# Optimization experiments

Hardware: AMD Instinct MI355X
Metric: run time of the kernel (lower is better)

## Reference

```python
import jax, jax.numpy as jnp
import numpy as np

N_NODES = 100000
N_EDGES = 3200000
IN_FEATS = 512
EDGE_FEATS = 24
OUT_FEATS = 512
LN_EPS = 1e-5


def setup_inputs() -> dict:
    key = jax.random.key(0)
    ks = jax.random.split(key, 8)
    h = jax.random.normal(ks[0], (N_NODES, IN_FEATS), dtype=jnp.float32)
    m = jax.random.normal(ks[1], (N_EDGES, EDGE_FEATS), dtype=jnp.float32)
    dst = jax.random.randint(ks[2], (N_EDGES,), 0, N_NODES, dtype=jnp.int32)
    norm = jax.random.uniform(ks[3], (N_NODES, 1), dtype=jnp.float32)
    stdv = 1.0 / np.sqrt(IN_FEATS + EDGE_FEATS)
    W = jax.random.uniform(ks[4], (OUT_FEATS, IN_FEATS + EDGE_FEATS), dtype=jnp.float32, minval=-stdv, maxval=stdv)
    b = jax.random.uniform(ks[5], (OUT_FEATS,), dtype=jnp.float32, minval=-stdv, maxval=stdv)
    gamma = jnp.ones((OUT_FEATS,), dtype=jnp.float32)
    beta = jnp.zeros((OUT_FEATS,), dtype=jnp.float32)
    return {"h": h, "m": m, "dst": dst, "norm": norm, "W": W, "b": b, "gamma": gamma, "beta": beta}


def reference(h, m, dst, norm, W, b, gamma, beta):
    # copy_e + sum: segment-sum edge features into destination nodes -> [N, 24]
    ah = jax.ops.segment_sum(m, dst, num_segments=N_NODES)
    # scale by per-node norm, concat with node features -> [N, in+24]
    x = jnp.concatenate([h, ah * norm], axis=1)
    # linear
    y = jnp.einsum('nd,od->no', x, W) + b
    # layernorm (elementwise affine)
    mu = jnp.mean(y, axis=-1, keepdims=True)
    var = jnp.mean((y - mu) ** 2, axis=-1, keepdims=True)
    y = gamma * (y - mu) * jax.lax.rsqrt(var + LN_EPS) + beta
    # activation = relu
    return jax.nn.relu(y)
```

## Files before the change

### kernel.cpp

```cpp
#include <hip/hip_runtime.h>
#include <hip/hip_bf16.h>
#include <stdint.h>

#define NN 100000
#define NE 3200000
#define EF 24
#define KF 536
#define BM 64

typedef __attribute__((ext_vector_type(8))) short bf16x8;
typedef __attribute__((ext_vector_type(4))) float f32x4;

__device__ __forceinline__ unsigned short f2bf(float f) {
  union { float f; unsigned int u; } v; v.f = f;
  unsigned int r = v.u + 0x7FFFu + ((v.u >> 16) & 1u);
  return (unsigned short)(r >> 16);
}

__device__ __forceinline__ void gload_lds16(const void* g, void* l) {
  __builtin_amdgcn_global_load_lds(
      (const __attribute__((address_space(1))) unsigned int*)g,
      (__attribute__((address_space(3))) unsigned int*)l, 16, 0, 0);
}

__global__ void wconv_kernel(const float* __restrict__ W, unsigned short* __restrict__ Wb) {
  int i = blockIdx.x * blockDim.x + threadIdx.x;
  if (i >= 17 * 32 * 64 * 8) return;
  int j = i & 7;
  int lane = (i >> 3) & 63;
  int nt = (i >> 9) & 31;
  int kt = i >> 14;
  int row = nt * 16 + (lane & 15);
  int k = kt * 32 + (lane >> 4) * 8 + j;
  float v = (k < KF) ? W[row * KF + k] : 0.0f;
  Wb[i] = f2bf(v);
}

__global__ __launch_bounds__(256) void init_u64_kernel(unsigned long long* __restrict__ acc) {
  int i = blockIdx.x * 256 + threadIdx.x;
  if (i < NN * 6) acc[i] = 0x4000400040004000ULL;
}

__global__ __launch_bounds__(256) void scatter_u64_kernel(
    const float* __restrict__ m, const int* __restrict__ dst,
    unsigned long long* __restrict__ acc) {
  int i = blockIdx.x * 256 + threadIdx.x;
  if (i >= NE * 6) return;
  int e = i / 6;
  int fp = i - e * 6;
  float4 v = *(const float4*)(m + (size_t)e * EF + fp * 4);
  long long a0 = (long long)__float2int_rn(v.x * 128.f);
  long long a1 = (long long)__float2int_rn(v.y * 128.f);
  long long a2 = (long long)__float2int_rn(v.z * 128.f);
  long long a3 = (long long)__float2int_rn(v.w * 128.f);
  unsigned long long add = (unsigned long long)(a0 + (a1 << 16) + (a2 << 32) + (a3 << 48));
  atomicAdd(acc + (size_t)dst[e] * 6 + fp, add);
}

__global__ __launch_bounds__(256) void decode_u64_kernel(
    const unsigned long long* __restrict__ acc, const float* __restrict__ norm,
    float* __restrict__ ah) {
  int i = blockIdx.x * 256 + threadIdx.x;
  if (i >= NN * 6) return;
  int n = i / 6;
  unsigned long long x = acc[i];
  float nv = norm[n] * (1.0f / 128.0f);
  float4 o;
  o.x = (float)((int)((x >> 0) & 0xFFFF) - 16384) * nv;
  o.y = (float)((int)((x >> 16) & 0xFFFF) - 16384) * nv;
  o.z = (float)((int)((x >> 32) & 0xFFFF) - 16384) * nv;
  o.w = (float)((int)((x >> 48) & 0xFFFF) - 16384) * nv;
  *(float4*)(ah + (size_t)i * 4) = o;
}

__global__ __launch_bounds__(512, 4) void gemm_ln_kernel(
    const float* __restrict__ h, const float* __restrict__ ah,
    const unsigned short* __restrict__ Wb,
    const float* __restrict__ bias, const float* __restrict__ gamma,
    const float* __restrict__ beta, float* __restrict__ out) {
  __shared__ __align__(16) unsigned short Alds[4 * 4 * 16 * 8];
  __shared__ __align__(16) unsigned short Blds[32 * 4 * 16 * 8];
  __shared__ float red[4][BM][2];
  __shared__ float stats[BM][2];

  const int t = threadIdx.x;
  const int lane = t & 63;
  const int w = t >> 6;
  const int lgrp = lane >> 4;
  const int llow = lane & 15;
  const int mg = w >> 2;
  const int ng = w & 3;
  const int blockRow = blockIdx.x * BM;

  const int am = t >> 3;
  const int akg = (t >> 1) & 3;
  const int ahalf = t & 1;
  const int arow = blockRow + am;
  char* aldsdst = (char*)Alds + (((am >> 4) * 64 + akg * 16 + (am & 15)) * 16 + ahalf * 8);

  f32x4 acc[2][8];
#pragma unroll
  for (int i = 0; i < 2; ++i)
#pragma unroll
    for (int j = 0; j < 8; ++j) acc[i][j] = (f32x4){0.f, 0.f, 0.f, 0.f};

  float4 ra = make_float4(0.f, 0.f, 0.f, 0.f);
  if (arow < NN) ra = *(const float4*)(h + (size_t)arow * 512 + akg * 8 + ahalf * 4);

  for (int kt = 0; kt < 17; ++kt) {
    {
      const unsigned short* src = Wb + ((size_t)(kt * 32 + w) * 64 + lane) * 8;
#pragma unroll
      for (int j = 0; j < 4; ++j)
        gload_lds16(src + (size_t)j * 8 * 64 * 8, (char*)Blds + (j * 8 + w) * 1024);
    }
    {
      ushort4 bv;
      bv.x = f2bf(ra.x); bv.y = f2bf(ra.y); bv.z = f2bf(ra.z); bv.w = f2bf(ra.w);
      *(ushort4*)aldsdst = bv;
    }
    ra = make_float4(0.f, 0.f, 0.f, 0.f);
    if (kt < 16 && arow < NN) {
      if (kt < 15) {
        ra = *(const float4*)(h + (size_t)arow * 512 + (kt + 1) * 32 + akg * 8 + ahalf * 4);
      } else if (akg < 3) {
        ra = *(const float4*)(ah + (size_t)arow * EF + akg * 8 + ahalf * 4);
      }
    }
    __syncthreads();

    bf16x8 af0 = *(const bf16x8*)((const char*)Alds + (((mg * 2 + 0) * 64) + lane) * 16);
    bf16x8 af1 = *(const bf16x8*)((const char*)Alds + (((mg * 2 + 1) * 64) + lane) * 16);
#pragma unroll
    for (int j = 0; j < 8; ++j) {
      int nt = ng * 8 + j;
      bf16x8 bf = *(const bf16x8*)((const char*)Blds + ((nt * 64) + lane) * 16);
      acc[0][j] = __builtin_amdgcn_mfma_f32_16x16x32_bf16(af0, bf, acc[0][j], 0, 0, 0);
      acc[1][j] = __builtin_amdgcn_mfma_f32_16x16x32_bf16(af1, bf, acc[1][j], 0, 0, 0);
    }
    __syncthreads();
  }

  float bcol[8], gcol[8], btcol[8];
#pragma unroll
  for (int j = 0; j < 8; ++j) {
    int col = (ng * 8 + j) * 16 + llow;
    bcol[j] = bias[col];
    gcol[j] = gamma[col];
    btcol[j] = beta[col];
  }
  float s[2][4], ss[2][4];
#pragma unroll
  for (int mt = 0; mt < 2; ++mt)
#pragma unroll
    for (int r = 0; r < 4; ++r) { s[mt][r] = 0.f; ss[mt][r] = 0.f; }
#pragma unroll
  for (int mt = 0; mt < 2; ++mt)
#pragma unroll
    for (int j = 0; j < 8; ++j)
#pragma unroll
      for (int r = 0; r < 4; ++r) {
        float v = acc[mt][j][r] + bcol[j];
        acc[mt][j][r] = v;
        s[mt][r] += v;
        ss[mt][r] += v * v;
      }
#pragma unroll
  for (int off = 1; off < 16; off <<= 1) {
#pragma unroll
    for (int mt = 0; mt < 2; ++mt)
#pragma unroll
      for (int r = 0; r < 4; ++r) {
        s[mt][r] += __shfl_xor(s[mt][r], off, 64);
        ss[mt][r] += __shfl_xor(ss[mt][r], off, 64);
      }
  }
  if (llow == 0) {
#pragma unroll
    for (int mt = 0; mt < 2; ++mt)
#pragma unroll
      for (int r = 0; r < 4; ++r) {
        int lrow = (mg * 2 + mt) * 16 + lgrp * 4 + r;
        red[ng][lrow][0] = s[mt][r];
        red[ng][lrow][1] = ss[mt][r];
      }
  }
  __syncthreads();
  if (t < BM) {
    float sum = red[0][t][0] + red[1][t][0] + red[2][t][0] + red[3][t][0];
    float sq = red[0][t][1] + red[1][t][1] + red[2][t][1] + red[3][t][1];
    float mean = sum * (1.0f / 512.0f);
    float var = sq * (1.0f / 512.0f) - mean * mean;
    stats[t][0] = mean;
    stats[t][1] = rsqrtf(var + 1e-5f);
  }
  __syncthreads();
#pragma unroll
  for (int mt = 0; mt < 2; ++mt) {
#pragma unroll
    for (int r = 0; r < 4; ++r) {
      int lrow = (mg * 2 + mt) * 16 + lgrp * 4 + r;
      int grow = blockRow + lrow;
      if (grow < NN) {
        float mean = stats[lrow][0];
        float rstd = stats[lrow][1];
#pragma unroll
        for (int j = 0; j < 8; ++j) {
          int col = (ng * 8 + j) * 16 + llow;
          float v = (acc[mt][j][r] - mean) * rstd * gcol[j] + btcol[j];
          out[grow * 512 + col] = fmaxf(v, 0.0f);
        }
      }
    }
  }
}

extern "C" void kernel_launch(void* const* d_in, const int* in_sizes, int n_in,
                              void* d_out, int out_size, void* d_ws, size_t ws_size,
                              hipStream_t stream) {
  const float* h = (const float*)d_in[0];
  const float* m = (const float*)d_in[1];
  const int* dst = (const int*)d_in[2];
  const float* norm = (const float*)d_in[3];
  const float* W = (const float*)d_in[4];
  const float* b = (const float*)d_in[5];
  const float* gamma = (const float*)d_in[6];
  const float* beta = (const float*)d_in[7];
  float* out = (float*)d_out;

  float* ah = (float*)d_ws;
  unsigned short* Wb = (unsigned short*)((char*)d_ws + 9600000);

  unsigned long long* acc = (unsigned long long*)d_out;

  init_u64_kernel<<<(NN * 6 + 255) / 256, 256, 0, stream>>>(acc);
  wconv_kernel<<<(17 * 32 * 64 * 8 + 255) / 256, 256, 0, stream>>>(W, Wb);
  scatter_u64_kernel<<<(NE * 6 + 255) / 256, 256, 0, stream>>>(m, dst, acc);
  decode_u64_kernel<<<(NN * 6 + 255) / 256, 256, 0, stream>>>(acc, norm, ah);
  gemm_ln_kernel<<<(NN + BM - 1) / BM, 512, 0, stream>>>(h, ah, Wb, b, gamma, beta, out);
}
```

Baseline: 380.7 us.

## Double K-step per iteration in GEMM-LN kernel to halve barriers

After: 361.0 us. -5.2%, faster.

```diff
diff --git a/kernel.cpp b/kernel.cpp
--- a/kernel.cpp
+++ b/kernel.cpp
@@ -9,6 +9,7 @@
 #define BM 64
 
 typedef __attribute__((ext_vector_type(8))) short bf16x8;
+typedef __attribute__((ext_vector_type(8))) unsigned short u16x8;
 typedef __attribute__((ext_vector_type(4))) float f32x4;
 
 __device__ __forceinline__ unsigned short f2bf(float f) {
@@ -78,8 +79,8 @@
     const unsigned short* __restrict__ Wb,
     const float* __restrict__ bias, const float* __restrict__ gamma,
     const float* __restrict__ beta, float* __restrict__ out) {
-  __shared__ __align__(16) unsigned short Alds[4 * 4 * 16 * 8];
-  __shared__ __align__(16) unsigned short Blds[32 * 4 * 16 * 8];
+  __shared__ __align__(16) unsigned short Alds[2 * 2048];
+  __shared__ __align__(16) unsigned short Blds[2 * 16384];
   __shared__ float red[4][BM][2];
   __shared__ float stats[BM][2];
 
@@ -93,10 +94,11 @@
   const int blockRow = blockIdx.x * BM;
 
   const int am = t >> 3;
-  const int akg = (t >> 1) & 3;
-  const int ahalf = t & 1;
+  const int c = t & 7;
+  const int kkw = c >> 2;
+  const int akg = c & 3;
   const int arow = blockRow + am;
-  char* aldsdst = (char*)Alds + (((am >> 4) * 64 + akg * 16 + (am & 15)) * 16 + ahalf * 8);
+  char* aldsdst = (char*)Alds + kkw * 4096 + (((am >> 4) * 64 + akg * 16 + (am & 15)) * 16);
 
   f32x4 acc[2][8];
 #pragma unroll
@@ -104,31 +106,68 @@
 #pragma unroll
     for (int j = 0; j < 8; ++j) acc[i][j] = (f32x4){0.f, 0.f, 0.f, 0.f};
 
-  float4 ra = make_float4(0.f, 0.f, 0.f, 0.f);
-  if (arow < NN) ra = *(const float4*)(h + (size_t)arow * 512 + akg * 8 + ahalf * 4);
-
-  for (int kt = 0; kt < 17; ++kt) {
+  float4 ra0 = make_float4(0.f, 0.f, 0.f, 0.f), ra1 = ra0;
+  if (arow < NN) {
+    const float* p = h + (size_t)arow * 512 + c * 8;
+    ra0 = *(const float4*)p;
+    ra1 = *(const float4*)(p + 4);
+  }
+
+  for (int step = 0; step < 8; ++step) {
+#pragma unroll
+    for (int kk = 0; kk < 2; ++kk) {
+      const unsigned short* src = Wb + ((size_t)((step * 2 + kk) * 32 + w) * 64 + lane) * 8;
+#pragma unroll
+      for (int j = 0; j < 4; ++j)
+        gload_lds16(src + (size_t)j * 8 * 64 * 8, (char*)Blds + kk * 32768 + (j * 8 + w) * 1024);
+    }
     {
-      const unsigned short* src = Wb + ((size_t)(kt * 32 + w) * 64 + lane) * 8;
-#pragma unroll
-      for (int j = 0; j < 4; ++j)
-        gload_lds16(src + (size_t)j * 8 * 64 * 8, (char*)Blds + (j * 8 + w) * 1024);
-    }
-    {
-      ushort4 bv;
-      bv.x = f2bf(ra.x); bv.y = f2bf(ra.y); bv.z = f2bf(ra.z); bv.w = f2bf(ra.w);
-      *(ushort4*)aldsdst = bv;
-    }
-    ra = make_float4(0.f, 0.f, 0.f, 0.f);
-    if (kt < 16 && arow < NN) {
-      if (kt < 15) {
-        ra = *(const float4*)(h + (size_t)arow * 512 + (kt + 1) * 32 + akg * 8 + ahalf * 4);
-      } else if (akg < 3) {
-        ra = *(const float4*)(ah + (size_t)arow * EF + akg * 8 + ahalf * 4);
+      u16x8 bv;
+      bv[0] = f2bf(ra0.x); bv[1] = f2bf(ra0.y); bv[2] = f2bf(ra0.z); bv[3] = f2bf(ra0.w);
+      bv[4] = f2bf(ra1.x); bv[5] = f2bf(ra1.y); bv[6] = f2bf(ra1.z); bv[7] = f2bf(ra1.w);
+      *(u16x8*)aldsdst = bv;
+    }
+    ra0 = make_float4(0.f, 0.f, 0.f, 0.f); ra1 = ra0;
+    if (arow < NN) {
+      if (step < 7) {
+        const float* p = h + (size_t)arow * 512 + (step + 1) * 64 + c * 8;
+        ra0 = *(const float4*)p;
+        ra1 = *(const float4*)(p + 4);
+      } else if (c < 3) {
+        const float* p = ah + (size_t)arow * EF + c * 8;
+        ra0 = *(const float4*)p;
+        ra1 = *(const float4*)(p + 4);
       }
     }
     __syncthreads();
 
+#pragma unroll
+    for (int kk = 0; kk < 2; ++kk) {
+      bf16x8 af0 = *(const bf16x8*)((const char*)Alds + kk * 4096 + (((mg * 2 + 0) * 64) + lane) * 16);
+      bf16x8 af1 = *(const bf16x8*)((const char*)Alds + kk * 4096 + (((mg * 2 + 1) * 64) + lane) * 16);
+#pragma unroll
+      for (int j = 0; j < 8; ++j) {
+        int nt = ng * 8 + j;
+        bf16x8 bf = *(const bf16x8*)((const char*)Blds + kk * 32768 + ((nt * 64) + lane) * 16);
+        acc[0][j] = __builtin_amdgcn_mfma_f32_16x16x32_bf16(af0, bf, acc[0][j], 0, 0, 0);
+        acc[1][j] = __builtin_amdgcn_mfma_f32_16x16x32_bf16(af1, bf, acc[1][j], 0, 0, 0);
+      }
+    }
+    __syncthreads();
+  }
+
+  {
+    const unsigned short* src = Wb + ((size_t)(16 * 32 + w) * 64 + lane) * 8;
+#pragma unroll
+    for (int j = 0; j < 4; ++j)
+      gload_lds16(src + (size_t)j * 8 * 64 * 8, (char*)Blds + (j * 8 + w) * 1024);
+    if (c < 4) {
+      u16x8 bv;
+      bv[0] = f2bf(ra0.x); bv[1] = f2bf(ra0.y); bv[2] = f2bf(ra0.z); bv[3] = f2bf(ra0.w);
+      bv[4] = f2bf(ra1.x); bv[5] = f2bf(ra1.y); bv[6] = f2bf(ra1.z); bv[7] = f2bf(ra1.w);
+      *(u16x8*)((char*)Alds + (((am >> 4) * 64 + akg * 16 + (am & 15)) * 16)) = bv;
+    }
+    __syncthreads();
     bf16x8 af0 = *(const bf16x8*)((const char*)Alds + (((mg * 2 + 0) * 64) + lane) * 16);
     bf16x8 af1 = *(const bf16x8*)((const char*)Alds + (((mg * 2 + 1) * 64) + lane) * 16);
 #pragma unroll
@@ -138,7 +177,6 @@
       acc[0][j] = __builtin_amdgcn_mfma_f32_16x16x32_bf16(af0, bf, acc[0][j], 0, 0, 0);
       acc[1][j] = __builtin_amdgcn_mfma_f32_16x16x32_bf16(af1, bf, acc[1][j], 0, 0, 0);
     }
-    __syncthreads();
   }
 
   float bcol[8], gcol[8], btcol[8];
```
